# Performance work log

Hardware: AMD Instinct MI355X
Metric: run time of the kernel (lower is better)

Reference implementation:

```python
import jax, jax.numpy as jnp
import numpy as np

N = 100000


def _gcn_prep(edge_index, n):
    # add self-loops, compute symmetric normalization (PyG gcn_norm defaults)
    loops = jnp.arange(n, dtype=edge_index.dtype)
    src = jnp.concatenate([edge_index[0], loops])
    dst = jnp.concatenate([edge_index[1], loops])
    deg = jax.ops.segment_sum(jnp.ones_like(src, dtype=jnp.float32), dst, num_segments=n)
    dinv = jnp.where(deg > 0, jax.lax.rsqrt(deg), 0.0)
    norm = dinv[src] * dinv[dst]  # [E + n]
    return src, dst, norm


def _gcn_layer(x, W, b, src, dst, norm, n):
    h = x @ W                              # [n, out]
    msgs = h[src] * norm[:, None]          # gather + scale, [E+n, out]
    agg = jax.ops.segment_sum(msgs, dst, num_segments=n)
    return agg + b


def setup_inputs() -> dict:
    key = jax.random.key(0)
    ks = jax.random.split(key, 8)
    E = 3200000
    x = jax.random.normal(ks[0], (N, 1), dtype=jnp.float32)
    edge_index = jax.random.randint(ks[1], (2, E), 0, N, dtype=jnp.int64)
    W1 = jax.random.normal(ks[2], (1, 16), dtype=jnp.float32) * (1.0 / np.sqrt(1))
    b1 = jax.random.normal(ks[3], (16,), dtype=jnp.float32) * 0.01
    W2 = jax.random.normal(ks[4], (16, 8), dtype=jnp.float32) * (1.0 / np.sqrt(16))
    b2 = jax.random.normal(ks[5], (8,), dtype=jnp.float32) * 0.01
    Wfc = jax.random.normal(ks[6], (8, 1), dtype=jnp.float32) * (1.0 / np.sqrt(8))
    bfc = jax.random.normal(ks[7], (1,), dtype=jnp.float32) * 0.01
    return {"x": x, "edge_index": edge_index, "W1": W1, "b1": b1,
            "W2": W2, "b2": b2, "Wfc": Wfc, "bfc": bfc}


def reference(x, edge_index, W1, b1, W2, b2, Wfc, bfc):
    n = x.shape[0]
    src, dst, norm = _gcn_prep(edge_index, n)
    h = jax.nn.relu(_gcn_layer(x, W1, b1, src, dst, norm, n))   # [N, 16]
    h = jax.nn.relu(_gcn_layer(h, W2, b2, src, dst, norm, n))   # [N, 8]
    out = h[-1] @ Wfc + bfc                                     # fc applied to last node only
    return out
```

## Files before the change

### kernel.cpp

```cpp
#include <hip/hip_runtime.h>


#define S1CAP 2048
#define DCAP  192
#define L2CAP 65536
#define HASHSZ 512

__global__ __launch_bounds__(256)
void k_pass1(const int* __restrict__ src, const int* __restrict__ dst,
             int E4, int E, int n, int* __restrict__ cnts,
             int* __restrict__ S1, unsigned* __restrict__ bm1,
             int* __restrict__ Dlist) {
    int i = blockIdx.x * blockDim.x + threadIdx.x;
    const int tgt = n - 1;
    if (i < E4) {
        int4 d4 = ((const int4*)dst)[i];
        int dd[4] = {d4.x, d4.y, d4.z, d4.w};
#pragma unroll
        for (int k = 0; k < 4; ++k) {
            if (dd[k] == tgt) {
                int s = src[i * 4 + k];
                int p = atomicAdd(&cnts[0], 1);
                if (p < S1CAP) S1[p] = s;
                unsigned bit = 1u << (s & 31);
                unsigned old = atomicOr(&bm1[s >> 5], bit);
                if (!(old & bit)) {
                    int q = atomicAdd(&cnts[1], 1);
                    if (q < DCAP) Dlist[q] = s;
                }
            }
        }
    }
    if (i == 0) {
        for (int e = E4 * 4; e < E; ++e) {
            if (dst[e] == tgt) {
                int s = src[e];
                int p = atomicAdd(&cnts[0], 1);
                if (p < S1CAP) S1[p] = s;
                unsigned bit = 1u << (s & 31);
                unsigned old = atomicOr(&bm1[s >> 5], bit);
                if (!(old & bit)) {
                    int q = atomicAdd(&cnts[1], 1);
                    if (q < DCAP) Dlist[q] = s;
                }
            }
        }
        unsigned bit = 1u << (tgt & 31);
        unsigned old = atomicOr(&bm1[tgt >> 5], bit);
        if (!(old & bit)) {
            int q = atomicAdd(&cnts[1], 1);
            if (q < DCAP) Dlist[q] = tgt;
        }
    }
}

__global__ __launch_bounds__(256)
void k_pass2(const int* __restrict__ src, const int* __restrict__ dst,
             int E4, int E, const unsigned* __restrict__ bm1,
             int* __restrict__ cnts, unsigned long long* __restrict__ L2,
             unsigned* __restrict__ bm2, int* __restrict__ deg,
             const int* __restrict__ Dlist) {
    int i = blockIdx.x * blockDim.x + threadIdx.x;
    if (i < DCAP) {
        int cntD = cnts[1]; if (cntD > DCAP) cntD = DCAP;
        if (i < cntD) {
            int d = Dlist[i];
            unsigned bit = 1u << (d & 31);
            unsigned old = atomicOr(&bm2[d >> 5], bit);
            if (!(old & bit)) deg[d] = 0;
        }
    }
    if (i < E4) {
        int4 d4 = ((const int4*)dst)[i];
        int dd[4] = {d4.x, d4.y, d4.z, d4.w};
#pragma unroll
        for (int k = 0; k < 4; ++k) {
            int d = dd[k];
            if ((bm1[d >> 5] >> (d & 31)) & 1u) {
                int s = src[i * 4 + k];
                int p = atomicAdd(&cnts[2], 1);
                if (p < L2CAP)
                    L2[p] = ((unsigned long long)(unsigned)d << 32) | (unsigned)s;
                unsigned bit = 1u << (s & 31);
                unsigned old = atomicOr(&bm2[s >> 5], bit);
                if (!(old & bit)) deg[s] = 0;
            }
        }
    }
    if (i == 0) {
        for (int e = E4 * 4; e < E; ++e) {
            int d = dst[e];
            if ((bm1[d >> 5] >> (d & 31)) & 1u) {
                int s = src[e];
                int p = atomicAdd(&cnts[2], 1);
                if (p < L2CAP)
                    L2[p] = ((unsigned long long)(unsigned)d << 32) | (unsigned)s;
                unsigned bit = 1u << (s & 31);
                unsigned old = atomicOr(&bm2[s >> 5], bit);
                if (!(old & bit)) deg[s] = 0;
            }
        }
    }
}

__global__ __launch_bounds__(256)
void k_pass3(const int* __restrict__ dst, int E4, int E,
             const unsigned* __restrict__ bm2, int* __restrict__ deg) {
    int i = blockIdx.x * blockDim.x + threadIdx.x;
    if (i < E4) {
        int4 d4 = ((const int4*)dst)[i];
        int dd[4] = {d4.x, d4.y, d4.z, d4.w};
#pragma unroll
        for (int k = 0; k < 4; ++k) {
            int d = dd[k];
            if ((bm2[d >> 5] >> (d & 31)) & 1u) atomicAdd(&deg[d], 1);
        }
    }
    if (i == 0) {
        for (int e = E4 * 4; e < E; ++e) {
            int d = dst[e];
            if ((bm2[d >> 5] >> (d & 31)) & 1u) atomicAdd(&deg[d], 1);
        }
    }
}

__global__ __launch_bounds__(256)
void k_final(const float* __restrict__ x, const int* __restrict__ deg,
             const int* __restrict__ cnts, const int* __restrict__ S1,
             const int* __restrict__ Dlist,
             const unsigned long long* __restrict__ L2,
             const float* __restrict__ W1, const float* __restrict__ b1,
             const float* __restrict__ W2, const float* __restrict__ b2,
             const float* __restrict__ Wfc, const float* __restrict__ bfc,
             int n, float* __restrict__ out) {
    __shared__ int hKey[HASHSZ];
    __shared__ int hVal[HASHSZ];
    __shared__ int sD[DCAP];
    __shared__ float s1D[DCAP];
    __shared__ float gD[DCAP][8];
    __shared__ float sW1[16], sb1[16], sW2[128], agg[8];

    const int tid = threadIdx.x;
    const int tgt = n - 1;
    int cnt1 = cnts[0]; if (cnt1 > S1CAP) cnt1 = S1CAP;
    int cntD = cnts[1]; if (cntD > DCAP) cntD = DCAP;
    int cnt2 = cnts[2]; if (cnt2 > L2CAP) cnt2 = L2CAP;

    for (int i = tid; i < HASHSZ; i += 256) hKey[i] = -1;
    for (int i = tid; i < cntD; i += 256) { sD[i] = Dlist[i]; s1D[i] = 0.f; }
    if (tid < 16) { sW1[tid] = W1[tid]; sb1[tid] = b1[tid]; }
    if (tid < 128) sW2[tid] = W2[tid];
    if (tid < 8) agg[tid] = 0.f;
    __syncthreads();
    for (int i = tid; i < cntD; i += 256) {
        int d = sD[i];
        int h = d & (HASHSZ - 1);
        while (true) {
            int prev = atomicCAS(&hKey[h], -1, d);
            if (prev == -1 || prev == d) { hVal[h] = i; break; }
            h = (h + 1) & (HASHSZ - 1);
        }
    }
    __syncthreads();
    for (int e = tid; e < cnt2; e += 256) {
        unsigned long long v = L2[e];
        int s = (int)(v & 0xffffffffu);
        int d = (int)(v >> 32);
        float msg = x[s] * rsqrtf((float)(deg[s] + 1));
        int h = d & (HASHSZ - 1);
        while (hKey[h] != d) h = (h + 1) & (HASHSZ - 1);
        atomicAdd(&s1D[hVal[h]], msg);
    }
    __syncthreads();
    for (int di = tid; di < cntD; di += 256) {
        int d = sD[di];
        float dv = rsqrtf((float)(deg[d] + 1));
        float t = dv * (s1D[di] + x[d] * dv);
        float g8[8] = {0, 0, 0, 0, 0, 0, 0, 0};
#pragma unroll
        for (int c = 0; c < 16; ++c) {
            float h1 = fmaxf(fmaf(t, sW1[c], sb1[c]), 0.f);
#pragma unroll
            for (int j = 0; j < 8; ++j) g8[j] = fmaf(h1, sW2[c * 8 + j], g8[j]);
        }
#pragma unroll
        for (int j = 0; j < 8; ++j) gD[di][j] = dv * g8[j];
    }
    __syncthreads();
    for (int idx = tid; idx < cnt1 * 8; idx += 256) {
        int p = idx >> 3, j = idx & 7;
        int s = S1[p];
        int h = s & (HASHSZ - 1);
        while (hKey[h] != s) h = (h + 1) & (HASHSZ - 1);
        atomicAdd(&agg[j], gD[hVal[h]][j]);
    }
    __syncthreads();
    if (tid == 0) {
        int h = tgt & (HASHSZ - 1);
        while (hKey[h] != tgt) h = (h + 1) & (HASHSZ - 1);
        int it = hVal[h];
        float dv = rsqrtf((float)(deg[tgt] + 1));
        float o = 0.f;
#pragma unroll
        for (int j = 0; j < 8; ++j)
            o += fmaxf(fmaf(dv, agg[j] + gD[it][j], b2[j]), 0.f) * Wfc[j];
        out[0] = o + bfc[0];
    }
}

extern "C" void kernel_launch(void* const* d_in, const int* in_sizes, int n_in,
                              void* d_out, int out_size, void* d_ws, size_t ws_size,
                              hipStream_t stream) {
    const float* x   = (const float*)d_in[0];
    const int*   ei  = (const int*)d_in[1];
    const float* W1  = (const float*)d_in[2];
    const float* b1  = (const float*)d_in[3];
    const float* W2  = (const float*)d_in[4];
    const float* b2  = (const float*)d_in[5];
    const float* Wfc = (const float*)d_in[6];
    const float* bfc = (const float*)d_in[7];
    float* out = (float*)d_out;

    int n = in_sizes[0];
    int E = in_sizes[1] / 2;
    const int* src = ei;
    const int* dst = ei + E;

    auto align16 = [](size_t v) { return (v + 15) & ~(size_t)15; };
    size_t bmBytes = align16(((size_t)(n + 31) / 32) * 4);
    char* ws = (char*)d_ws;
    size_t off = 0;
    unsigned* bm1   = (unsigned*)(ws + off); off += bmBytes;
    unsigned* bm2   = (unsigned*)(ws + off); off += bmBytes;
    int*      cnts  = (int*)(ws + off);      off += 64;
    size_t zeroBytes = off;
    int*      deg   = (int*)(ws + off);      off += align16((size_t)n * 4);
    int*      S1    = (int*)(ws + off);      off += S1CAP * 4;
    int*      Dlist = (int*)(ws + off);      off += align16(DCAP * 4);
    unsigned long long* L2 = (unsigned long long*)(ws + off); off += (size_t)L2CAP * 8;

    hipMemsetAsync(d_ws, 0, zeroBytes, stream);

    int E4 = E >> 2;
    int bE4 = (E4 + 255) / 256;

    k_pass1<<<bE4, 256, 0, stream>>>(src, dst, E4, E, n, cnts, S1, bm1, Dlist);
    k_pass2<<<bE4, 256, 0, stream>>>(src, dst, E4, E, bm1, cnts, L2, bm2, deg, Dlist);
    k_pass3<<<bE4, 256, 0, stream>>>(dst, E4, E, bm2, deg);
    k_final<<<1,   256, 0, stream>>>(x, deg, cnts, S1, Dlist, L2,
                                     W1, b1, W2, b2, Wfc, bfc, n, out);
}
```

Baseline: 117.8 us.

## Replace global bitmap with per-block shared hash, fuse final into pass3 via last-block

Pass1 now only collects in-neighbors of the target, dropping the bitmap and dedup atomics. Pass2 builds a per-block shared-memory hash of those neighbors and probes it instead of reading a global bitmap, and writes bm2/deg without dedup checks. The single-block final kernel is folded into pass3 using a last-block-done counter, which saves a launch. The trade is a rebuilt hash in every block and extra fences.

```diff
diff --git a/kernel.cpp b/kernel.cpp
--- a/kernel.cpp
+++ b/kernel.cpp
@@ -4,13 +4,13 @@
 #define S1CAP 2048
 #define DCAP  192
 #define L2CAP 65536
-#define HASHSZ 512
+#define HASHD 4096
+#define HASHF 512
 
 __global__ __launch_bounds__(256)
 void k_pass1(const int* __restrict__ src, const int* __restrict__ dst,
              int E4, int E, int n, int* __restrict__ cnts,
-             int* __restrict__ S1, unsigned* __restrict__ bm1,
-             int* __restrict__ Dlist) {
+             int* __restrict__ S1) {
     int i = blockIdx.x * blockDim.x + threadIdx.x;
     const int tgt = n - 1;
     if (i < E4) {
@@ -22,12 +22,6 @@
                 int s = src[i * 4 + k];
                 int p = atomicAdd(&cnts[0], 1);
                 if (p < S1CAP) S1[p] = s;
-                unsigned bit = 1u << (s & 31);
-                unsigned old = atomicOr(&bm1[s >> 5], bit);
-                if (!(old & bit)) {
-                    int q = atomicAdd(&cnts[1], 1);
-                    if (q < DCAP) Dlist[q] = s;
-                }
             }
         }
     }
@@ -37,76 +31,95 @@
                 int s = src[e];
                 int p = atomicAdd(&cnts[0], 1);
                 if (p < S1CAP) S1[p] = s;
-                unsigned bit = 1u << (s & 31);
-                unsigned old = atomicOr(&bm1[s >> 5], bit);
-                if (!(old & bit)) {
-                    int q = atomicAdd(&cnts[1], 1);
-                    if (q < DCAP) Dlist[q] = s;
-                }
-            }
-        }
-        unsigned bit = 1u << (tgt & 31);
-        unsigned old = atomicOr(&bm1[tgt >> 5], bit);
-        if (!(old & bit)) {
-            int q = atomicAdd(&cnts[1], 1);
-            if (q < DCAP) Dlist[q] = tgt;
+            }
         }
     }
 }
 
 __global__ __launch_bounds__(256)
 void k_pass2(const int* __restrict__ src, const int* __restrict__ dst,
-             int E4, int E, const unsigned* __restrict__ bm1,
-             int* __restrict__ cnts, unsigned long long* __restrict__ L2,
-             unsigned* __restrict__ bm2, int* __restrict__ deg,
-             const int* __restrict__ Dlist) {
-    int i = blockIdx.x * blockDim.x + threadIdx.x;
-    if (i < DCAP) {
-        int cntD = cnts[1]; if (cntD > DCAP) cntD = DCAP;
-        if (i < cntD) {
-            int d = Dlist[i];
-            unsigned bit = 1u << (d & 31);
-            unsigned old = atomicOr(&bm2[d >> 5], bit);
-            if (!(old & bit)) deg[d] = 0;
-        }
-    }
+             int E4, int E, int n, int* __restrict__ cnts,
+             const int* __restrict__ S1, unsigned long long* __restrict__ L2,
+             unsigned* __restrict__ bm2, int* __restrict__ deg) {
+    __shared__ int dKey[HASHD];
+    const int tid = threadIdx.x;
+    const int tgt = n - 1;
+    for (int j = tid; j < HASHD; j += 256) dKey[j] = -1;
+    __syncthreads();
+    int cnt1 = cnts[0]; if (cnt1 > S1CAP) cnt1 = S1CAP;
+    for (int j = tid; j < cnt1 + 1; j += 256) {
+        int d = (j < cnt1) ? S1[j] : tgt;
+        int h = d & (HASHD - 1);
+        while (true) {
+            int prev = atomicCAS(&dKey[h], -1, d);
+            if (prev == -1 || prev == d) break;
+            h = (h + 1) & (HASHD - 1);
+        }
+    }
+    __syncthreads();
+    if (blockIdx.x == 0) {
+        for (int j = tid; j < cnt1 + 1; j += 256) {
+            int d = (j < cnt1) ? S1[j] : tgt;
+            atomicOr(&bm2[d >> 5], 1u << (d & 31));
+            deg[d] = 0;
+        }
+    }
+    int i = blockIdx.x * blockDim.x + tid;
     if (i < E4) {
         int4 d4 = ((const int4*)dst)[i];
         int dd[4] = {d4.x, d4.y, d4.z, d4.w};
 #pragma unroll
         for (int k = 0; k < 4; ++k) {
             int d = dd[k];
-            if ((bm1[d >> 5] >> (d & 31)) & 1u) {
+            int h = d & (HASHD - 1);
+            int key;
+            while ((key = dKey[h]) != -1 && key != d) h = (h + 1) & (HASHD - 1);
+            if (key == d) {
                 int s = src[i * 4 + k];
                 int p = atomicAdd(&cnts[2], 1);
                 if (p < L2CAP)
                     L2[p] = ((unsigned long long)(unsigned)d << 32) | (unsigned)s;
-                unsigned bit = 1u << (s & 31);
-                unsigned old = atomicOr(&bm2[s >> 5], bit);
-                if (!(old & bit)) deg[s] = 0;
+                atomicOr(&bm2[s >> 5], 1u << (s & 31));
+                deg[s] = 0;
             }
         }
     }
     if (i == 0) {
         for (int e = E4 * 4; e < E; ++e) {
             int d = dst[e];
-            if ((bm1[d >> 5] >> (d & 31)) & 1u) {
+            int h = d & (HASHD - 1);
+            int key;
+            while ((key = dKey[h]) != -1 && key != d) h = (h + 1) & (HASHD - 1);
+            if (key == d) {
                 int s = src[e];
                 int p = atomicAdd(&cnts[2], 1);
                 if (p < L2CAP)
                     L2[p] = ((unsigned long long)(unsigned)d << 32) | (unsigned)s;
-                unsigned bit = 1u << (s & 31);
-                unsigned old = atomicOr(&bm2[s >> 5], bit);
-                if (!(old & bit)) deg[s] = 0;
-            }
-        }
-    }
+                atomicOr(&bm2[s >> 5], 1u << (s & 31));
+                deg[s] = 0;
+            }
+        }
+    }
+}
+
+__device__ __forceinline__ int deg_load(const int* p) {
+    return __hip_atomic_load(p, __ATOMIC_RELAXED, __HIP_MEMORY_SCOPE_AGENT);
 }
 
 __global__ __launch_bounds__(256)
-void k_pass3(const int* __restrict__ dst, int E4, int E,
-             const unsigned* __restrict__ bm2, int* __restrict__ deg) {
-    int i = blockIdx.x * blockDim.x + threadIdx.x;
+void k_pass3(const float* __restrict__ x, const int* __restrict__ dst,
+             int E4, int E, int n, int* __restrict__ cnts,
+             const int* __restrict__ S1,
+             const unsigned long long* __restrict__ L2,
+             const unsigned* __restrict__ bm2, int* __restrict__ deg,
+             int* __restrict__ done,
+             const float* __restrict__ W1, const float* __restrict__ b1,
+             const float* __restrict__ W2, const float* __restrict__ b2,
+             const float* __restrict__ Wfc, const float* __restrict__ bfc,
+             float* __restrict__ out) {
+    const int tid = threadIdx.x;
+    const int tgt = n - 1;
+    int i = blockIdx.x * blockDim.x + tid;
     if (i < E4) {
         int4 d4 = ((const int4*)dst)[i];
         int dd[4] = {d4.x, d4.y, d4.z, d4.w};
@@ -122,59 +135,67 @@
             if ((bm2[d >> 5] >> (d & 31)) & 1u) atomicAdd(&deg[d], 1);
         }
     }
-}
-
-__global__ __launch_bounds__(256)
-void k_final(const float* __restrict__ x, const int* __restrict__ deg,
-             const int* __restrict__ cnts, const int* __restrict__ S1,
-             const int* __restrict__ Dlist,
-             const unsigned long long* __restrict__ L2,
-             const float* __restrict__ W1, const float* __restrict__ b1,
-             const float* __restrict__ W2, const float* __restrict__ b2,
-             const float* __restrict__ Wfc, const float* __restrict__ bfc,
-             int n, float* __restrict__ out) {
-    __shared__ int hKey[HASHSZ];
-    __shared__ int hVal[HASHSZ];
+    __shared__ int amLast;
+    __syncthreads();
+    __threadfence();
+    if (tid == 0) {
+        int prev = atomicAdd(done, 1);
+        amLast = (prev == (int)gridDim.x - 1);
+    }
+    __syncthreads();
+    if (!amLast) return;
+    __threadfence();
+
+    __shared__ int hKey[HASHF];
+    __shared__ int hVal[HASHF];
     __shared__ int sD[DCAP];
     __shared__ float s1D[DCAP];
     __shared__ float gD[DCAP][8];
     __shared__ float sW1[16], sb1[16], sW2[128], agg[8];
-
-    const int tid = threadIdx.x;
-    const int tgt = n - 1;
+    __shared__ int nD;
+
     int cnt1 = cnts[0]; if (cnt1 > S1CAP) cnt1 = S1CAP;
-    int cntD = cnts[1]; if (cntD > DCAP) cntD = DCAP;
     int cnt2 = cnts[2]; if (cnt2 > L2CAP) cnt2 = L2CAP;
 
-    for (int i = tid; i < HASHSZ; i += 256) hKey[i] = -1;
-    for (int i = tid; i < cntD; i += 256) { sD[i] = Dlist[i]; s1D[i] = 0.f; }
+    for (int j = tid; j < HASHF; j += 256) hKey[j] = -1;
     if (tid < 16) { sW1[tid] = W1[tid]; sb1[tid] = b1[tid]; }
     if (tid < 128) sW2[tid] = W2[tid];
     if (tid < 8) agg[tid] = 0.f;
-    __syncthreads();
-    for (int i = tid; i < cntD; i += 256) {
-        int d = sD[i];
-        int h = d & (HASHSZ - 1);
+    if (tid == 0) nD = 0;
+    __syncthreads();
+    for (int j = tid; j < cnt1 + 1; j += 256) {
+        int d = (j < cnt1) ? S1[j] : tgt;
+        int h = d & (HASHF - 1);
         while (true) {
             int prev = atomicCAS(&hKey[h], -1, d);
-            if (prev == -1 || prev == d) { hVal[h] = i; break; }
-            h = (h + 1) & (HASHSZ - 1);
-        }
-    }
+            if (prev == -1) {
+                int q = atomicAdd(&nD, 1);
+                if (q >= DCAP) q = 0;
+                hVal[h] = q;
+                sD[q] = d;
+                break;
+            }
+            if (prev == d) break;
+            h = (h + 1) & (HASHF - 1);
+        }
+    }
+    __syncthreads();
+    int cntD = nD; if (cntD > DCAP) cntD = DCAP;
+    for (int j = tid; j < cntD; j += 256) s1D[j] = 0.f;
     __syncthreads();
     for (int e = tid; e < cnt2; e += 256) {
         unsigned long long v = L2[e];
         int s = (int)(v & 0xffffffffu);
         int d = (int)(v >> 32);
-        float msg = x[s] * rsqrtf((float)(deg[s] + 1));
-        int h = d & (HASHSZ - 1);
-        while (hKey[h] != d) h = (h + 1) & (HASHSZ - 1);
+        float msg = x[s] * rsqrtf((float)(deg_load(&deg[s]) + 1));
+        int h = d & (HASHF - 1);
+        while (hKey[h] != d) h = (h + 1) & (HASHF - 1);
         atomicAdd(&s1D[hVal[h]], msg);
     }
     __syncthreads();
     for (int di = tid; di < cntD; di += 256) {
         int d = sD[di];
-        float dv = rsqrtf((float)(deg[d] + 1));
+        float dv = rsqrtf((float)(deg_load(&deg[d]) + 1));
         float t = dv * (s1D[di] + x[d] * dv);
         float g8[8] = {0, 0, 0, 0, 0, 0, 0, 0};
 #pragma unroll
@@ -190,16 +211,16 @@
     for (int idx = tid; idx < cnt1 * 8; idx += 256) {
         int p = idx >> 3, j = idx & 7;
         int s = S1[p];
-        int h = s & (HASHSZ - 1);
-        while (hKey[h] != s) h = (h + 1) & (HASHSZ - 1);
+        int h = s & (HASHF - 1);
+        while (hKey[h] != s) h = (h + 1) & (HASHF - 1);
         atomicAdd(&agg[j], gD[hVal[h]][j]);
     }
     __syncthreads();
     if (tid == 0) {
-        int h = tgt & (HASHSZ - 1);
-        while (hKey[h] != tgt) h = (h + 1) & (HASHSZ - 1);
+        int h = tgt & (HASHF - 1);
+        while (hKey[h] != tgt) h = (h + 1) & (HASHF - 1);
         int it = hVal[h];
-        float dv = rsqrtf((float)(deg[tgt] + 1));
+        float dv = rsqrtf((float)(deg_load(&deg[tgt]) + 1));
         float o = 0.f;
 #pragma unroll
         for (int j = 0; j < 8; ++j)
@@ -230,13 +251,12 @@
     size_t bmBytes = align16(((size_t)(n + 31) / 32) * 4);
     char* ws = (char*)d_ws;
     size_t off = 0;
-    unsigned* bm1   = (unsigned*)(ws + off); off += bmBytes;
-    unsigned* bm2   = (unsigned*)(ws + off); off += bmBytes;
-    int*      cnts  = (int*)(ws + off);      off += 64;
+    unsigned* bm2  = (unsigned*)(ws + off); off += bmBytes;
+    int*      cnts = (int*)(ws + off);      off += 64;
+    int*      done = (int*)(ws + off);      off += 64;
     size_t zeroBytes = off;
-    int*      deg   = (int*)(ws + off);      off += align16((size_t)n * 4);
-    int*      S1    = (int*)(ws + off);      off += S1CAP * 4;
-    int*      Dlist = (int*)(ws + off);      off += align16(DCAP * 4);
+    int*      deg  = (int*)(ws + off);      off += align16((size_t)n * 4);
+    int*      S1   = (int*)(ws + off);      off += S1CAP * 4;
     unsigned long long* L2 = (unsigned long long*)(ws + off); off += (size_t)L2CAP * 8;
 
     hipMemsetAsync(d_ws, 0, zeroBytes, stream);
@@ -244,9 +264,8 @@
     int E4 = E >> 2;
     int bE4 = (E4 + 255) / 256;
 
-    k_pass1<<<bE4, 256, 0, stream>>>(src, dst, E4, E, n, cnts, S1, bm1, Dlist);
-    k_pass2<<<bE4, 256, 0, stream>>>(src, dst, E4, E, bm1, cnts, L2, bm2, deg, Dlist);
-    k_pass3<<<bE4, 256, 0, stream>>>(dst, E4, E, bm2, deg);
-    k_final<<<1,   256, 0, stream>>>(x, deg, cnts, S1, Dlist, L2,
-                                     W1, b1, W2, b2, Wfc, bfc, n, out);
-}
+    k_pass1<<<bE4, 256, 0, stream>>>(src, dst, E4, E, n, cnts, S1);
+    k_pass2<<<bE4, 256, 0, stream>>>(src, dst, E4, E, n, cnts, S1, L2, bm2, deg);
+    k_pass3<<<bE4, 256, 0, stream>>>(x, dst, E4, E, n, cnts, S1, L2, bm2, deg,
+                                     done, W1, b1, W2, b2, Wfc, bfc, out);
+}
```

Result: slower. 295.9 us (+151.1%).
